# Kernel tuning notes

Measured on AMD Instinct MI355X. Metric: run time of the kernel, lower is better.

The kernel has to match this reference:

```python
import jax, jax.numpy as jnp
import numpy as np

LATENT_DIM = 8
POLY_DEGREE = 5
DATA_DIM = 64
BATCH = 4096
TOTAL_TERMS = sum(LATENT_DIM ** d for d in range(POLY_DEGREE + 1))  # 37449


def _poly_features(z):
    # z: [B, L] -> [B, sum_d L^d] concatenated Kronecker powers, degree 0..D.
    B = z.shape[0]
    feats = [jnp.ones((B, 1), dtype=z.dtype)]  # degree 0
    cur = z  # degree 1: [B, L]
    feats.append(cur)
    for _ in range(2, POLY_DEGREE + 1):
        # kron(cur, z) per sample: outer product then flatten (row-major matches torch.kron)
        cur = (cur[:, :, None] * z[:, None, :]).reshape(B, -1)
        feats.append(cur)
    return jnp.concatenate(feats, axis=1)  # [B, TOTAL_TERMS]


def setup_inputs() -> dict:
    key = jax.random.key(0)
    k1, k2, k3 = jax.random.split(key, 3)
    z = jax.random.normal(k1, (BATCH, LATENT_DIM), dtype=jnp.float32)
    W = jax.random.normal(k2, (DATA_DIM, TOTAL_TERMS), dtype=jnp.float32) / np.sqrt(TOTAL_TERMS)
    b = jax.random.normal(k3, (DATA_DIM,), dtype=jnp.float32)
    return {"z": z, "W": W, "b": b}


def reference(z, W, b):
    feats = _poly_features(z)                 # [B, TOTAL_TERMS]
    return feats @ W.T + b                    # [B, DATA_DIM]
```

## Files before the change

kernel.cpp:

```cpp
#include <hip/hip_runtime.h>


#define TOTAL_TERMS 37449
#define NSTEP 1172
#define MBLK 32
#define KY 21
#define OUT_ELEMS 262144

typedef _Float16 half8 __attribute__((ext_vector_type(8)));
typedef float f32x4 __attribute__((ext_vector_type(4)));

__global__ __launch_bounds__(256) void convert_w(const float* __restrict__ W,
                                                 const float* __restrict__ bias,
                                                 _Float16* __restrict__ Wt) {
    __shared__ _Float16 lds[64][72];
    int tid  = threadIdx.x;
    int lane = tid & 63;
    int nq   = tid >> 6;
    int kb   = blockIdx.x * 64;
    int kp   = kb + lane;

    int o, mode;
    if (kp < 8)           { o = 1 + kp;            mode = 0; }
    else if (kp == 8)     { o = 0;                 mode = 2; }
    else if (kp < 32)     { o = 0;                 mode = 1; }
    else if (kp < 96)     { o = 9    + (kp - 32);  mode = 0; }
    else if (kp < 608)    { o = 73   + (kp - 96);  mode = 0; }
    else if (kp < 4704)   { o = 585  + (kp - 608); mode = 0; }
    else if (kp < 37472)  { o = 4681 + (kp - 4704);mode = 0; }
    else                  { o = 0;                 mode = 1; }

#pragma unroll
    for (int r = 0; r < 16; ++r) {
        int n = r * 4 + nq;
        const float* wrow = W + (size_t)n * TOTAL_TERMS;
        float v;
        if (mode == 1)      v = 0.f;
        else if (mode == 2) v = wrow[0] + bias[n];
        else                v = wrow[o];
        lds[n][lane] = (_Float16)v;
    }
    __syncthreads();

    int quad = lane >> 4, l16 = lane & 15;
    int n = nq * 16 + l16;
#pragma unroll
    for (int sl = 0; sl < 2; ++sl) {
        int kk = sl * 32 + quad * 8;
        half8 hv;
#pragma unroll
        for (int j = 0; j < 8; ++j) hv[j] = lds[n][kk + j];
        int s = (kb >> 5) + sl;
        *(half8*)(Wt + ((size_t)(s * 4 + nq) * 64 + lane) * 8) = hv;
    }
}

__global__ __launch_bounds__(256, 4) void poly_gemm(const float* __restrict__ z,
                                                    const _Float16* __restrict__ Wt,
                                                    float* __restrict__ part,
                                                    float* __restrict__ out,
                                                    int use_atomic) {
    __shared__ __align__(16) _Float16 zm[128][8];
    __shared__ _Float16 zT[8][144];

    int tid  = threadIdx.x;
    int lane = tid & 63;
    int w    = tid >> 6;
    int g    = w >> 1;
    int h    = w & 1;
    int mb   = blockIdx.x;
    int ky   = blockIdx.y;

    if (tid < 128) {
        const float* zp = z + ((size_t)(mb * 128 + tid)) * 8;
        float4 a = *(const float4*)zp;
        float4 b4 = *(const float4*)(zp + 4);
        half8 hz;
        hz[0] = (_Float16)a.x;  hz[1] = (_Float16)a.y;
        hz[2] = (_Float16)a.z;  hz[3] = (_Float16)a.w;
        hz[4] = (_Float16)b4.x; hz[5] = (_Float16)b4.y;
        hz[6] = (_Float16)b4.z; hz[7] = (_Float16)b4.w;
        *(half8*)&zm[tid][0] = hz;
#pragma unroll
        for (int j = 0; j < 8; ++j) zT[j][tid] = hz[j];
    }
    __syncthreads();

    int quad = lane >> 4;
    int l16  = lane & 15;
    int mrow[4];
    half8 zv[4];
    _Float16 zq[4], zq4[4];
#pragma unroll
    for (int t = 0; t < 4; ++t) {
        mrow[t] = g * 64 + t * 16 + l16;
        zv[t]   = *(const half8*)&zm[mrow[t]][0];
        zq[t]   = zT[quad][mrow[t]];
        zq4[t]  = zT[quad + 4][mrow[t]];
    }

    f32x4 acc[4][2];
#pragma unroll
    for (int t = 0; t < 4; ++t)
#pragma unroll
        for (int k = 0; k < 2; ++k) acc[t][k] = (f32x4){0.f, 0.f, 0.f, 0.f};

    const _Float16* base = Wt + (size_t)h * 1024 + (size_t)lane * 8;

    auto loadB = [&](int s, half8* B) {
        const _Float16* p = base + (size_t)s * 2048;
        B[0] = *(const half8*)p;
        B[1] = *(const half8*)(p + 512);
    };
    auto mfma8 = [&](const half8* av, const half8* B) {
#pragma unroll
        for (int t = 0; t < 4; ++t)
#pragma unroll
            for (int k = 0; k < 2; ++k)
                acc[t][k] = __builtin_amdgcn_mfma_f32_16x16x32_f16(
                    av[t], B[k], acc[t][k], 0, 0, 0);
    };

    if (ky < 20) {
        const bool d5 = (ky < 16);
        const int  nh16   = d5 ? 4 : 2;
        const int  sbase  = d5 ? (147 + 64 * ky) : (19 + 32 * (ky - 16));
        const int  r2base = d5 ? (4 * ky) : (2 * (ky - 16));

        _Float16 a1[4];
        if (d5) {
            int r1 = (ky >> 1) & 7;
#pragma unroll
            for (int t = 0; t < 4; ++t) a1[t] = zT[r1][mrow[t]];
        }

        half8 B0[2], B1[2];
        loadB(sbase, B0);
        loadB(sbase + 1, B1);

        for (int h16 = 0; h16 < nh16; ++h16) {
            int r2 = (r2base + h16) & 7;
            _Float16 gz[4];
#pragma unroll
            for (int t = 0; t < 4; ++t) {
                _Float16 v = zT[r2][mrow[t]];
                gz[t] = d5 ? (_Float16)(a1[t] * v) : v;
            }
            int sh = sbase + h16 * 16;
#pragma unroll
            for (int i2 = 0; i2 < 16; i2 += 2) {
                half8 av[4];
#pragma unroll
                for (int t = 0; t < 4; ++t) {
                    _Float16 f = gz[t] * zv[t][i2 >> 1] * zq[t];
#pragma unroll
                    for (int e = 0; e < 8; ++e) av[t][e] = zv[t][e] * f;
                }
                mfma8(av, B0);
                loadB(sh + i2 + 2, B0);
#pragma unroll
                for (int t = 0; t < 4; ++t) {
                    _Float16 f = gz[t] * zv[t][i2 >> 1] * zq4[t];
#pragma unroll
                    for (int e = 0; e < 8; ++e) av[t][e] = zv[t][e] * f;
                }
                mfma8(av, B1);
                loadB(sh + i2 + 3, B1);
            }
        }
    } else {
        auto genA = [&](int s, half8* av) {
            if (s == 0) {
#pragma unroll
                for (int t = 0; t < 4; ++t) {
                    if (quad == 0)      av[t] = zv[t];
                    else if (quad == 1) { av[t] = (half8){}; av[t][0] = (_Float16)1.f; }
                    else                av[t] = (half8){};
                }
                return;
            }
            _Float16 f[4];
            if (s >= 3) {
                int u = s - 3;
                int r1 = (u >> 1) & 7;
                int r2 = ((u & 1) << 2) + quad;
#pragma unroll
                for (int t = 0; t < 4; ++t)
                    f[t] = zT[r1][mrow[t]] * zT[r2][mrow[t]];
            } else {
                int r1 = (s - 1) * 4 + quad;
#pragma unroll
                for (int t = 0; t < 4; ++t)
                    f[t] = zT[r1][mrow[t]];
            }
#pragma unroll
            for (int t = 0; t < 4; ++t)
#pragma unroll
                for (int e = 0; e < 8; ++e) av[t][e] = zv[t][e] * f[t];
        };

        half8 B0[2], B1[2];
        loadB(0, B0);
        loadB(1, B1);
        int s = 0;
        for (; s + 1 < 19; s += 2) {
            half8 av[4];
            genA(s, av);
            mfma8(av, B0);
            if (s + 2 < 19) loadB(s + 2, B0);
            genA(s + 1, av);
            mfma8(av, B1);
            if (s + 3 < 19) loadB(s + 3, B1);
        }
        {
            half8 av[4];
            genA(18, av);
            mfma8(av, B0);
        }
    }

    float* dstbase = use_atomic ? out : (part + (size_t)ky * OUT_ELEMS);
#pragma unroll
    for (int t = 0; t < 4; ++t) {
        int mbase = mb * 128 + g * 64 + t * 16 + quad * 4;
#pragma unroll
        for (int k = 0; k < 2; ++k) {
            int col = h * 32 + k * 16 + l16;
#pragma unroll
            for (int r = 0; r < 4; ++r) {
                size_t idx = (size_t)(mbase + r) * 64 + col;
                if (use_atomic) unsafeAtomicAdd(dstbase + idx, acc[t][k][r]);
                else            dstbase[idx] = acc[t][k][r];
            }
        }
    }
}

__global__ __launch_bounds__(256) void reduce_part(const float* __restrict__ part,
                                                   float* __restrict__ out) {
    int gid = blockIdx.x * 256 + threadIdx.x;
    const f32x4* p4 = (const f32x4*)part;
    f32x4 s = (f32x4){0.f, 0.f, 0.f, 0.f};
#pragma unroll
    for (int j = 0; j < KY; ++j)
        s += p4[(size_t)j * (OUT_ELEMS / 4) + gid];
    ((f32x4*)out)[gid] = s;
}

extern "C" void kernel_launch(void* const* d_in, const int* in_sizes, int n_in,
                              void* d_out, int out_size, void* d_ws, size_t ws_size,
                              hipStream_t stream) {
    (void)in_sizes; (void)n_in;
    const float* z = (const float*)d_in[0];
    const float* W = (const float*)d_in[1];
    const float* b = (const float*)d_in[2];
    float* out = (float*)d_out;

    const size_t part_bytes = (size_t)KY * OUT_ELEMS * sizeof(float);
    const size_t wt_bytes   = (size_t)(NSTEP + 2) * 2048 * sizeof(_Float16);
    const bool two_phase = ws_size >= part_bytes + wt_bytes;

    float* part;
    _Float16* Wt;
    if (two_phase) {
        part = (float*)d_ws;
        Wt   = (_Float16*)((char*)d_ws + part_bytes);
    } else {
        part = out;
        Wt   = (_Float16*)d_ws;
    }

    if (!two_phase)
        hipMemsetAsync(d_out, 0, (size_t)out_size * sizeof(float), stream);
    hipLaunchKernelGGL(convert_w, dim3(NSTEP / 2), dim3(256), 0, stream, W, b, Wt);
    hipLaunchKernelGGL(poly_gemm, dim3(MBLK, KY), dim3(256), 0, stream,
                       z, Wt, part, out, two_phase ? 0 : 1);
    if (two_phase)
        hipLaunchKernelGGL(reduce_part, dim3(OUT_ELEMS / 4 / 256), dim3(256), 0,
                           stream, part, out);
}
```

Before: 95.32 us.

## Stage W tiles into LDS via async global_load_lds double buffering

Replaces per-wave direct global loads of the fp16 W tiles with cooperative global_load_lds copies into a double-buffered 32KB LDS buffer, gated by block barriers. Each wave then reads its B fragments from LDS. Also swaps the grid axes so consecutive blocks walk K slices, and uses nontemporal stores/loads for the partial sums and the reduction. The added LDS footprint and per-chunk __syncthreads may reduce occupancy and add barrier stalls, and the workspace size grows slightly to cover staging overrun.

```diff
diff --git a/kernel.cpp b/kernel.cpp
--- a/kernel.cpp
+++ b/kernel.cpp
@@ -60,6 +60,7 @@
                                                     float* __restrict__ part,
                                                     float* __restrict__ out,
                                                     int use_atomic) {
+    __shared__ __align__(16) _Float16 bbuf[2][8192];
     __shared__ __align__(16) _Float16 zm[128][8];
     __shared__ _Float16 zT[8][144];
 
@@ -68,8 +69,8 @@
     int w    = tid >> 6;
     int g    = w >> 1;
     int h    = w & 1;
-    int mb   = blockIdx.x;
-    int ky   = blockIdx.y;
+    int ky   = blockIdx.x;
+    int mb   = blockIdx.y;
 
     if (tid < 128) {
         const float* zp = z + ((size_t)(mb * 128 + tid)) * 8;
@@ -105,10 +106,24 @@
 #pragma unroll
         for (int k = 0; k < 2; ++k) acc[t][k] = (f32x4){0.f, 0.f, 0.f, 0.f};
 
-    const _Float16* base = Wt + (size_t)h * 1024 + (size_t)lane * 8;
-
-    auto loadB = [&](int s, half8* B) {
-        const _Float16* p = base + (size_t)s * 2048;
+    const int sb = (ky < 16) ? (147 + 64 * ky)
+                 : (ky < 20) ? (19 + 32 * (ky - 16)) : 0;
+
+    auto stage = [&](int gc, int parity) {
+        int pbase = (sb + gc * 4) * 4;
+        _Float16* lb = &bbuf[parity][0];
+#pragma unroll
+        for (int i = 0; i < 4; ++i) {
+            int piece = w * 4 + i;
+            const _Float16* gp = Wt + ((size_t)(pbase + piece) << 9) + lane * 8;
+            __builtin_amdgcn_global_load_lds(
+                (const __attribute__((address_space(1))) void*)gp,
+                (__attribute__((address_space(3))) void*)(lb + piece * 512 + lane * 8),
+                16, 0, 0);
+        }
+    };
+    auto readB = [&](int parity, int ii, half8* B) {
+        const _Float16* p = &bbuf[parity][(ii * 4 + 2 * h) * 512 + lane * 8];
         B[0] = *(const half8*)p;
         B[1] = *(const half8*)(p + 512);
     };
@@ -122,10 +137,10 @@
     };
 
     if (ky < 20) {
-        const bool d5 = (ky < 16);
-        const int  nh16   = d5 ? 4 : 2;
-        const int  sbase  = d5 ? (147 + 64 * ky) : (19 + 32 * (ky - 16));
-        const int  r2base = d5 ? (4 * ky) : (2 * (ky - 16));
+        const bool d5     = (ky < 16);
+        const int  r2base = d5 ? 4 * ky : 2 * (ky - 16);
+        const int  nsc    = d5 ? 4 : 2;
+        const int  ntot   = nsc * 4;
 
         _Float16 a1[4];
         if (d5) {
@@ -134,38 +149,35 @@
             for (int t = 0; t < 4; ++t) a1[t] = zT[r1][mrow[t]];
         }
 
-        half8 B0[2], B1[2];
-        loadB(sbase, B0);
-        loadB(sbase + 1, B1);
-
-        for (int h16 = 0; h16 < nh16; ++h16) {
-            int r2 = (r2base + h16) & 7;
+        stage(0, 0);
+        for (int sc = 0; sc < nsc; ++sc) {
+            int rtop = (r2base + sc) & 7;
             _Float16 gz[4];
 #pragma unroll
             for (int t = 0; t < 4; ++t) {
-                _Float16 v = zT[r2][mrow[t]];
+                _Float16 v = zT[rtop][mrow[t]];
                 gz[t] = d5 ? (_Float16)(a1[t] * v) : v;
             }
-            int sh = sbase + h16 * 16;
-#pragma unroll
-            for (int i2 = 0; i2 < 16; i2 += 2) {
-                half8 av[4];
-#pragma unroll
-                for (int t = 0; t < 4; ++t) {
-                    _Float16 f = gz[t] * zv[t][i2 >> 1] * zq[t];
-#pragma unroll
-                    for (int e = 0; e < 8; ++e) av[t][e] = zv[t][e] * f;
+#pragma unroll
+            for (int cc = 0; cc < 4; ++cc) {
+                __syncthreads();
+                int gc = sc * 4 + cc;
+                if (gc + 1 < ntot) stage(gc + 1, (cc + 1) & 1);
+#pragma unroll
+                for (int ii = 0; ii < 4; ++ii) {
+                    half8 B[2];
+                    readB(cc & 1, ii, B);
+                    const int r3 = 2 * cc + (ii >> 1);
+                    half8 av[4];
+#pragma unroll
+                    for (int t = 0; t < 4; ++t) {
+                        _Float16 f = gz[t] * zv[t][r3] *
+                                     ((ii & 1) ? zq4[t] : zq[t]);
+#pragma unroll
+                        for (int e = 0; e < 8; ++e) av[t][e] = zv[t][e] * f;
+                    }
+                    mfma8(av, B);
                 }
-                mfma8(av, B0);
-                loadB(sh + i2 + 2, B0);
-#pragma unroll
-                for (int t = 0; t < 4; ++t) {
-                    _Float16 f = gz[t] * zv[t][i2 >> 1] * zq4[t];
-#pragma unroll
-                    for (int e = 0; e < 8; ++e) av[t][e] = zv[t][e] * f;
-                }
-                mfma8(av, B1);
-                loadB(sh + i2 + 3, B1);
             }
         }
     } else {
@@ -199,23 +211,18 @@
                 for (int e = 0; e < 8; ++e) av[t][e] = zv[t][e] * f[t];
         };
 
-        half8 B0[2], B1[2];
-        loadB(0, B0);
-        loadB(1, B1);
-        int s = 0;
-        for (; s + 1 < 19; s += 2) {
-            half8 av[4];
-            genA(s, av);
-            mfma8(av, B0);
-            if (s + 2 < 19) loadB(s + 2, B0);
-            genA(s + 1, av);
-            mfma8(av, B1);
-            if (s + 3 < 19) loadB(s + 3, B1);
-        }
-        {
-            half8 av[4];
-            genA(18, av);
-            mfma8(av, B0);
+        stage(0, 0);
+        for (int gc = 0; gc < 5; ++gc) {
+            __syncthreads();
+            if (gc + 1 < 5) stage(gc + 1, (gc + 1) & 1);
+            int nst = (gc == 4) ? 3 : 4;
+            for (int ii = 0; ii < nst; ++ii) {
+                half8 B[2];
+                readB(gc & 1, ii, B);
+                half8 av[4];
+                genA(gc * 4 + ii, av);
+                mfma8(av, B);
+            }
         }
     }
 
@@ -229,8 +236,8 @@
 #pragma unroll
             for (int r = 0; r < 4; ++r) {
                 size_t idx = (size_t)(mbase + r) * 64 + col;
-                if (use_atomic) unsafeAtomicAdd(dstbase + idx, acc[t][k][r]);
-                else            dstbase[idx] = acc[t][k][r];
+                if (use_atomic) unsafeAtomicAdd(out + idx, acc[t][k][r]);
+                else __builtin_nontemporal_store(acc[t][k][r], dstbase + idx);
             }
         }
     }
@@ -243,8 +250,8 @@
     f32x4 s = (f32x4){0.f, 0.f, 0.f, 0.f};
 #pragma unroll
     for (int j = 0; j < KY; ++j)
-        s += p4[(size_t)j * (OUT_ELEMS / 4) + gid];
-    ((f32x4*)out)[gid] = s;
+        s += __builtin_nontemporal_load(p4 + (size_t)j * (OUT_ELEMS / 4) + gid);
+    __builtin_nontemporal_store(s, ((f32x4*)out) + gid);
 }
 
 extern "C" void kernel_launch(void* const* d_in, const int* in_sizes, int n_in,
@@ -257,7 +264,7 @@
     float* out = (float*)d_out;
 
     const size_t part_bytes = (size_t)KY * OUT_ELEMS * sizeof(float);
-    const size_t wt_bytes   = (size_t)(NSTEP + 2) * 2048 * sizeof(_Float16);
+    const size_t wt_bytes   = (size_t)(NSTEP + 4) * 2048 * sizeof(_Float16);
     const bool two_phase = ws_size >= part_bytes + wt_bytes;
 
     float* part;
@@ -273,7 +280,7 @@
     if (!two_phase)
         hipMemsetAsync(d_out, 0, (size_t)out_size * sizeof(float), stream);
     hipLaunchKernelGGL(convert_w, dim3(NSTEP / 2), dim3(256), 0, stream, W, b, Wt);
-    hipLaunchKernelGGL(poly_gemm, dim3(MBLK, KY), dim3(256), 0, stream,
+    hipLaunchKernelGGL(poly_gemm, dim3(KY, MBLK), dim3(256), 0, stream,
                        z, Wt, part, out, two_phase ? 0 : 1);
     if (two_phase)
         hipLaunchKernelGGL(reduce_part, dim3(OUT_ELEMS / 4 / 256), dim3(256), 0,
```

New measurement: 98.56 us. +3.4%, slower.

## Double-buffer 16-step W tiles in registers for main GEMM loop

Applied to the files above, without the earlier changes.

The degree-4/5 path now prefetches a whole group of 8 steps (16 half8 fragments) of W into a register double buffer before computing on the previous group. The load is issued before the z staging and sync, and launch bounds drop to 2 blocks per SM to make room for the extra registers. Partial-sum stores and the reduction use nontemporal loads and stores. The deeper prefetch is meant to hide global-memory latency, at the cost of occupancy and possible register spills. The workspace is enlarged so the prefetch that runs past the last group stays in bounds.

```diff
diff --git a/kernel.cpp b/kernel.cpp
--- a/kernel.cpp
+++ b/kernel.cpp
@@ -55,7 +55,7 @@
     }
 }
 
-__global__ __launch_bounds__(256, 4) void poly_gemm(const float* __restrict__ z,
+__global__ __launch_bounds__(256, 2) void poly_gemm(const float* __restrict__ z,
                                                     const _Float16* __restrict__ Wt,
                                                     float* __restrict__ part,
                                                     float* __restrict__ out,
@@ -70,6 +70,21 @@
     int h    = w & 1;
     int mb   = blockIdx.x;
     int ky   = blockIdx.y;
+
+    const int sb = (ky < 16) ? (147 + 64 * ky)
+                 : (ky < 20) ? (19 + 32 * (ky - 16)) : 0;
+
+    const char* gb = (const char*)Wt + (size_t)(sb * 4 + 2 * h) * 1024
+                   + (size_t)lane * 16;
+
+    half8 Bk[2][16];
+    if (ky < 20) {
+#pragma unroll
+        for (int ii = 0; ii < 8; ++ii)
+#pragma unroll
+            for (int k = 0; k < 2; ++k)
+                Bk[0][ii * 2 + k] = *(const half8*)(gb + ii * 4096 + k * 1024);
+    }
 
     if (tid < 128) {
         const float* zp = z + ((size_t)(mb * 128 + tid)) * 8;
@@ -105,27 +120,10 @@
 #pragma unroll
         for (int k = 0; k < 2; ++k) acc[t][k] = (f32x4){0.f, 0.f, 0.f, 0.f};
 
-    const _Float16* base = Wt + (size_t)h * 1024 + (size_t)lane * 8;
-
-    auto loadB = [&](int s, half8* B) {
-        const _Float16* p = base + (size_t)s * 2048;
-        B[0] = *(const half8*)p;
-        B[1] = *(const half8*)(p + 512);
-    };
-    auto mfma8 = [&](const half8* av, const half8* B) {
-#pragma unroll
-        for (int t = 0; t < 4; ++t)
-#pragma unroll
-            for (int k = 0; k < 2; ++k)
-                acc[t][k] = __builtin_amdgcn_mfma_f32_16x16x32_f16(
-                    av[t], B[k], acc[t][k], 0, 0, 0);
-    };
-
     if (ky < 20) {
-        const bool d5 = (ky < 16);
-        const int  nh16   = d5 ? 4 : 2;
-        const int  sbase  = d5 ? (147 + 64 * ky) : (19 + 32 * (ky - 16));
-        const int  r2base = d5 ? (4 * ky) : (2 * (ky - 16));
+        const bool d5     = (ky < 16);
+        const int  r2base = d5 ? 4 * ky : 2 * (ky - 16);
+        const int  nsc    = d5 ? 4 : 2;
 
         _Float16 a1[4];
         if (d5) {
@@ -134,41 +132,51 @@
             for (int t = 0; t < 4; ++t) a1[t] = zT[r1][mrow[t]];
         }
 
-        half8 B0[2], B1[2];
-        loadB(sbase, B0);
-        loadB(sbase + 1, B1);
-
-        for (int h16 = 0; h16 < nh16; ++h16) {
-            int r2 = (r2base + h16) & 7;
+        for (int sc = 0; sc < nsc; ++sc) {
+            int rtop = (r2base + sc) & 7;
             _Float16 gz[4];
 #pragma unroll
             for (int t = 0; t < 4; ++t) {
-                _Float16 v = zT[r2][mrow[t]];
+                _Float16 v = zT[rtop][mrow[t]];
                 gz[t] = d5 ? (_Float16)(a1[t] * v) : v;
             }
-            int sh = sbase + h16 * 16;
-#pragma unroll
-            for (int i2 = 0; i2 < 16; i2 += 2) {
-                half8 av[4];
-#pragma unroll
-                for (int t = 0; t < 4; ++t) {
-                    _Float16 f = gz[t] * zv[t][i2 >> 1] * zq[t];
-#pragma unroll
-                    for (int e = 0; e < 8; ++e) av[t][e] = zv[t][e] * f;
+#pragma unroll
+            for (int gp = 0; gp < 2; ++gp) {
+                const char* gn = gb + 32768;
+#pragma unroll
+                for (int ii = 0; ii < 8; ++ii)
+#pragma unroll
+                    for (int k = 0; k < 2; ++k)
+                        Bk[gp ^ 1][ii * 2 + k] =
+                            *(const half8*)(gn + ii * 4096 + k * 1024);
+#pragma unroll
+                for (int ii = 0; ii < 8; ++ii) {
+                    const int r3 = gp * 4 + (ii >> 1);
+                    half8 av[4];
+#pragma unroll
+                    for (int t = 0; t < 4; ++t) {
+                        _Float16 f = gz[t] * zv[t][r3] *
+                                     ((ii & 1) ? zq4[t] : zq[t]);
+#pragma unroll
+                        for (int e = 0; e < 8; ++e) av[t][e] = zv[t][e] * f;
+                    }
+#pragma unroll
+                    for (int t = 0; t < 4; ++t)
+#pragma unroll
+                        for (int k = 0; k < 2; ++k)
+                            acc[t][k] = __builtin_amdgcn_mfma_f32_16x16x32_f16(
+                                av[t], Bk[gp][ii * 2 + k], acc[t][k], 0, 0, 0);
                 }
-                mfma8(av, B0);
-                loadB(sh + i2 + 2, B0);
-#pragma unroll
-                for (int t = 0; t < 4; ++t) {
-                    _Float16 f = gz[t] * zv[t][i2 >> 1] * zq4[t];
-#pragma unroll
-                    for (int e = 0; e < 8; ++e) av[t][e] = zv[t][e] * f;
-                }
-                mfma8(av, B1);
-                loadB(sh + i2 + 3, B1);
+                gb += 32768;
             }
         }
     } else {
+        const _Float16* base = Wt + (size_t)h * 1024 + (size_t)lane * 8;
+        auto loadB = [&](int s, half8* B) {
+            const _Float16* p = base + (size_t)s * 2048;
+            B[0] = *(const half8*)p;
+            B[1] = *(const half8*)(p + 512);
+        };
         auto genA = [&](int s, half8* av) {
             if (s == 0) {
 #pragma unroll
@@ -197,6 +205,14 @@
             for (int t = 0; t < 4; ++t)
 #pragma unroll
                 for (int e = 0; e < 8; ++e) av[t][e] = zv[t][e] * f[t];
+        };
+        auto mfma8 = [&](const half8* av, const half8* B) {
+#pragma unroll
+            for (int t = 0; t < 4; ++t)
+#pragma unroll
+                for (int k = 0; k < 2; ++k)
+                    acc[t][k] = __builtin_amdgcn_mfma_f32_16x16x32_f16(
+                        av[t], B[k], acc[t][k], 0, 0, 0);
         };
 
         half8 B0[2], B1[2];
@@ -229,8 +245,8 @@
 #pragma unroll
             for (int r = 0; r < 4; ++r) {
                 size_t idx = (size_t)(mbase + r) * 64 + col;
-                if (use_atomic) unsafeAtomicAdd(dstbase + idx, acc[t][k][r]);
-                else            dstbase[idx] = acc[t][k][r];
+                if (use_atomic) unsafeAtomicAdd(out + idx, acc[t][k][r]);
+                else __builtin_nontemporal_store(acc[t][k][r], dstbase + idx);
             }
         }
     }
@@ -243,8 +259,8 @@
     f32x4 s = (f32x4){0.f, 0.f, 0.f, 0.f};
 #pragma unroll
     for (int j = 0; j < KY; ++j)
-        s += p4[(size_t)j * (OUT_ELEMS / 4) + gid];
-    ((f32x4*)out)[gid] = s;
+        s += __builtin_nontemporal_load(p4 + (size_t)j * (OUT_ELEMS / 4) + gid);
+    __builtin_nontemporal_store(s, ((f32x4*)out) + gid);
 }
 
 extern "C" void kernel_launch(void* const* d_in, const int* in_sizes, int n_in,
@@ -257,7 +273,7 @@
     float* out = (float*)d_out;
 
     const size_t part_bytes = (size_t)KY * OUT_ELEMS * sizeof(float);
-    const size_t wt_bytes   = (size_t)(NSTEP + 2) * 2048 * sizeof(_Float16);
+    const size_t wt_bytes   = (size_t)(NSTEP + 16) * 2048 * sizeof(_Float16);
     const bool two_phase = ws_size >= part_bytes + wt_bytes;
 
     float* part;
```

Measured after the change: 94.73 us. No clear change (-0.6%).
